# Performance work log

Hardware: AMD Instinct MI355X
Metric: run time of the kernel (lower is better)

Reference implementation:

```python
import jax, jax.numpy as jnp
import numpy as np

NMS_THRE = 0.4
NEG = -1e30  # sentinel for sort key of suppressed boxes


def _iou_adjacency(boxes, nms_thre):
    # boxes: [N,4] in cxcywh -> xyxy, then dense IoU >= thre adjacency (no self loops)
    cx, cy, w, h = boxes[:, 0], boxes[:, 1], boxes[:, 2], boxes[:, 3]
    x1 = cx - w / 2
    y1 = cy - h / 2
    x2 = x1 + w
    y2 = y1 + h
    b = jnp.stack([x1, y1, x2, y2], axis=-1)  # [N,4]
    area = (x2 - x1) * (y2 - y1)
    lt = jnp.maximum(b[:, None, :2], b[None, :, :2])  # [N,N,2]
    rb = jnp.minimum(b[:, None, 2:], b[None, :, 2:])
    wh = jnp.clip(rb - lt, 0.0)
    inter = wh[..., 0] * wh[..., 1]
    iou = inter / (area[:, None] + area[None, :] - inter)
    n = boxes.shape[0]
    return (iou >= nms_thre) & (~jnp.eye(n, dtype=bool))


def _greedy_suppress(valid0, adj, scores):
    # Sequential greedy NMS over candidates in descending score order.
    # valid shrinks monotonically, and valid <= valid0 always, so clearing
    # neighbors via adj row exactly matches the torch loop (which only clears
    # neighbors that were initially valid -- already-false entries are no-ops).
    order = jnp.argsort(-scores)

    def body(k, valid):
        idx = order[k]
        return jnp.where(valid[idx], valid & (~adj[idx]), valid)

    return jax.lax.fori_loop(0, scores.shape[0], body, valid0)


def _per_class(pro_c, con_c, conf_c, adj):
    # scatter_max over adjacency: max of con over neighbors (0 if no neighbors,
    # matching torch_scatter's zero-init)
    adj_con = jnp.max(jnp.where(adj, con_c[None, :], 0.0), axis=1)
    valid0 = (pro_c >= conf_c) & (pro_c >= adj_con) & (pro_c >= con_c)
    return _greedy_suppress(valid0, adj, pro_c)


def _per_image(pro, con, boxes, scale, conf_thres):
    # pro/con: [N,C]; boxes: [N,4] cxcywh; scale: scalar; conf_thres: [C]
    adj = _iou_adjacency(boxes, NMS_THRE)
    survive = jax.vmap(_per_class, in_axes=(1, 1, 0, None))(pro, con, conf_thres, adj)  # [C,N]
    b = boxes * scale
    cx, cy, w, h = b[:, 0], b[:, 1], b[:, 2], b[:, 3]
    xyxy = jnp.stack([cx - 0.5 * w, cy - 0.5 * h, cx + 0.5 * w, cy + 0.5 * h], axis=-1)  # [N,4]
    scores = pro.T  # [C,N]
    C = scores.shape[0]
    bws = jnp.concatenate(
        [jnp.broadcast_to(xyxy[None], (C,) + xyxy.shape), scores[..., None]], axis=-1
    )  # [C,N,5]
    bws = bws * survive[..., None].astype(bws.dtype)  # zero out suppressed rows
    key = jnp.where(survive, scores, NEG)
    perm = jnp.argsort(-key, axis=1)  # per-class descending score order
    bws = jnp.take_along_axis(bws, perm[..., None], axis=1)
    mask = jnp.take_along_axis(survive, perm, axis=1)
    return bws, mask


def setup_inputs() -> dict:
    key = jax.random.key(0)
    k1, k2, k3, k4 = jax.random.split(key, 4)
    B, N, C = 4, 3600, 16
    return {
        "pro_max": jax.random.uniform(k1, (B, N, C), dtype=jnp.float32),
        "con_max": jax.random.uniform(k2, (B, N, C), dtype=jnp.float32),
        "pred_boxes": jax.random.uniform(k3, (B, N, 4), dtype=jnp.float32),
        "image_scales": jax.random.uniform(k4, (B,), dtype=jnp.float32),
        "conf_thres": jnp.zeros((C,), dtype=jnp.float32),
    }


def reference(pro_max, con_max, pred_boxes, image_scales, conf_thres):
    # Returns (boxes_with_scores [B,C,N,5] sorted per class by score desc,
    #          survive_mask [B,C,N] aligned with the sorted rows).
    return jax.vmap(_per_image, in_axes=(0, 0, 0, 0, None))(
        pro_max, con_max, pred_boxes, image_scales, conf_thres
    )
```

## Files before the change

### kernel.cpp

```cpp
#include <hip/hip_runtime.h>
#include <cstdint>

typedef unsigned long long u64;
typedef unsigned int u32;

#define B_ 4
#define N_ 3600
#define C_ 16
#define NW_ 57
#define NPAD_ 3648
#define RPW_ 4
#define RPB_ 16
#define HW0_ 1856
#define HW1_ 1792
#define CH_ 64
#define NT_ 512
#define NWV_ 8
#define RPWG_ 8

__global__ __launch_bounds__(256, 5) void k_adj(const float* __restrict__ boxes,
                                                u64* __restrict__ adj) {
#pragma clang fp contract(off)
    __shared__ float4 sbox[HW0_];
    const int tid  = threadIdx.x;
    const int lane = tid & 63;
    const int wv   = tid >> 6;
    const int g    = blockIdx.x;
    const int b    = g / (N_ / RPB_);
    const int r0   = (g % (N_ / RPB_)) * RPB_ + wv * RPW_;
    const size_t bN = (size_t)b * N_;

    float4 bi[RPW_];
    float  ai[RPW_];
#pragma unroll
    for (int r = 0; r < RPW_; ++r) {
        const float4 bx = reinterpret_cast<const float4*>(boxes)[bN + r0 + r];
        const float x1 = bx.x - bx.z * 0.5f;
        const float y1 = bx.y - bx.w * 0.5f;
        const float x2 = x1 + bx.z;
        const float y2 = y1 + bx.w;
        bi[r] = make_float4(x1, y1, x2, y2);
        ai[r] = (x2 - x1) * (y2 - y1);
    }
    const double MID = (double)0.4f - 0x1p-26;

    u64 row[RPW_];
#pragma unroll
    for (int r = 0; r < RPW_; ++r) row[r] = 0ull;

    int jbase = 0;
    for (int h = 0; h < 2; ++h) {
        const int cnt = h ? HW1_ : HW0_;
        __syncthreads();
        for (int jj = tid; jj < cnt; jj += 256) {
            const int j = jbase + jj;
            float x1 = 0.f, y1 = 0.f, x2 = 0.f, y2 = 0.f;
            if (j < N_) {
                const float4 bx = reinterpret_cast<const float4*>(boxes)[bN + j];
                x1 = bx.x - bx.z * 0.5f;
                y1 = bx.y - bx.w * 0.5f;
                x2 = x1 + bx.z;
                y2 = y1 + bx.w;
            }
            sbox[jj] = make_float4(x1, y1, x2, y2);
        }
        __syncthreads();

        const int twn = cnt >> 6;
        for (int tw = 0; tw < twn; ++tw) {
            const int tglob = (jbase >> 6) + tw;
            const int j     = jbase + tw * 64 + lane;
            const float4 bj = sbox[tw * 64 + lane];
            const float ajr = (bj.z - bj.x) * (bj.w - bj.y);
#pragma unroll
            for (int r = 0; r < RPW_; ++r) {
                const float ltx = fmaxf(bi[r].x, bj.x);
                const float lty = fmaxf(bi[r].y, bj.y);
                const float rbx = fminf(bi[r].z, bj.z);
                const float rby = fminf(bi[r].w, bj.w);
                const float whx = fmaxf(rbx - ltx, 0.0f);
                const float why = fmaxf(rby - lty, 0.0f);
                const float inter = whx * why;
                const float denom = (ai[r] + ajr) - inter;
                const int pred = ((double)inter > MID * (double)denom) && (j != r0 + r);
                const u64 m = __ballot(pred);
                if (lane == tglob) row[r] = m;
            }
        }
        jbase += cnt;
    }

#pragma unroll
    for (int r = 0; r < RPW_; ++r)
        if (lane < NW_) adj[(bN + r0 + r) * (size_t)NW_ + lane] = row[r];
}

__global__ __launch_bounds__(256) void k_acon(const u64* __restrict__ adj,
                                              const float* __restrict__ con,
                                              float* __restrict__ thr) {
    const int tid  = threadIdx.x;
    const int lane = tid & 63;
    const int wv   = tid >> 6;
    const int g    = blockIdx.x;
    const int b    = g / (N_ / 4);
    const int i    = (g % (N_ / 4)) * 4 + wv;
    const size_t bN = (size_t)b * N_;

    u64 w = (lane < NW_) ? adj[(bN + i) * (size_t)NW_ + lane] : 0ull;

    float cm[C_];
#pragma unroll
    for (int k = 0; k < C_; ++k) cm[k] = 0.0f;

    while (w) {
        const int bit = __builtin_ctzll(w); w &= w - 1;
        const int j   = lane * 64 + bit;
        const float4* cp = reinterpret_cast<const float4*>(con + (bN + j) * C_);
        const float4 c0 = cp[0], c1 = cp[1], c2 = cp[2], c3 = cp[3];
        cm[0]  = fmaxf(cm[0],  c0.x); cm[1]  = fmaxf(cm[1],  c0.y);
        cm[2]  = fmaxf(cm[2],  c0.z); cm[3]  = fmaxf(cm[3],  c0.w);
        cm[4]  = fmaxf(cm[4],  c1.x); cm[5]  = fmaxf(cm[5],  c1.y);
        cm[6]  = fmaxf(cm[6],  c1.z); cm[7]  = fmaxf(cm[7],  c1.w);
        cm[8]  = fmaxf(cm[8],  c2.x); cm[9]  = fmaxf(cm[9],  c2.y);
        cm[10] = fmaxf(cm[10], c2.z); cm[11] = fmaxf(cm[11], c2.w);
        cm[12] = fmaxf(cm[12], c3.x); cm[13] = fmaxf(cm[13], c3.y);
        cm[14] = fmaxf(cm[14], c3.z); cm[15] = fmaxf(cm[15], c3.w);
    }

#pragma unroll
    for (int off = 1; off < 64; off <<= 1) {
#pragma unroll
        for (int k = 0; k < C_; ++k) cm[k] = fmaxf(cm[k], __shfl_xor(cm[k], off));
    }
    if (lane == 0) {
        const float4* cp = reinterpret_cast<const float4*>(con + (bN + i) * C_);
        const float4 c0 = cp[0], c1 = cp[1], c2 = cp[2], c3 = cp[3];
        float4* o = reinterpret_cast<float4*>(thr + (bN + i) * C_);
        o[0] = make_float4(fmaxf(cm[0],  c0.x), fmaxf(cm[1],  c0.y),
                           fmaxf(cm[2],  c0.z), fmaxf(cm[3],  c0.w));
        o[1] = make_float4(fmaxf(cm[4],  c1.x), fmaxf(cm[5],  c1.y),
                           fmaxf(cm[6],  c1.z), fmaxf(cm[7],  c1.w));
        o[2] = make_float4(fmaxf(cm[8],  c2.x), fmaxf(cm[9],  c2.y),
                           fmaxf(cm[10], c2.z), fmaxf(cm[11], c2.w));
        o[3] = make_float4(fmaxf(cm[12], c3.x), fmaxf(cm[13], c3.y),
                           fmaxf(cm[14], c3.z), fmaxf(cm[15], c3.w));
    }
}

union OvT {
    u64 keys[4096];
    u64 srows[2][CH_][NW_];
};

__global__ __launch_bounds__(NT_) void k_nms(const float* __restrict__ pro,
                                             const float* __restrict__ thr,
                                             const float* __restrict__ conf,
                                             const u64* __restrict__ adj,
                                             const float* __restrict__ boxes,
                                             const float* __restrict__ scales,
                                             float* __restrict__ out) {
#pragma clang fp contract(off)
    __shared__ OvT ov;
    __shared__ u32 sidx[NPAD_];
    __shared__ u64 sintra[CH_];
    __shared__ u64 vmask[NW_];
    __shared__ u64 s_accept;
    __shared__ u32 slist[NPAD_];
    __shared__ u32 s_T;
    __shared__ u32 s_S;
    const int tid  = threadIdx.x;
    const int lane = tid & 63;
    const int wv   = tid >> 6;
    const int bc   = blockIdx.x;
    const int b    = bc / C_, c = bc % C_;
    const size_t bN = (size_t)b * N_;
    const float cf = conf[c];

    if (tid == 0) s_T = 0;
    __syncthreads();

    for (int t = wv; t < NW_; t += NWV_) {
        const int i = t * 64 + lane;
        int pred = 0;
        u32 pk = 0;
        if (i < N_) {
            const size_t off = (bN + i) * C_ + c;
            const float p = pro[off];
            pred = (p >= cf) && (p >= thr[off]);
            const u32 pb = __float_as_uint(p);
            pk = pb ^ ((pb >> 31) ? 0xFFFFFFFFu : 0x80000000u);
        }
        const u64 bm = __ballot(pred);
        if (lane == 0) vmask[t] = bm;
        u32 base = 0;
        if (lane == 0 && bm) base = atomicAdd(&s_T, (u32)__popcll(bm));
        base = (u32)__shfl((int)base, 0);
        if (pred) ov.keys[base + (u32)__popcll(bm & ((1ull << lane) - 1ull))] =
            (((u64)(~pk)) << 32) | (u32)i;
    }
    __syncthreads();

    const int T = (int)s_T;
    int P = 2;
    while (P < T) P <<= 1;
    for (int x = T + tid; x < P; x += NT_) ov.keys[x] = ~0ull;
    __syncthreads();

    for (int k = 2; k <= P; k <<= 1) {
        for (int j = k >> 1; j > 0; j >>= 1) {
            for (int t = tid; t < P; t += NT_) {
                const int ixj = t ^ j;
                if (ixj > t) {
                    const u64 a = ov.keys[t], bb = ov.keys[ixj];
                    const bool up = ((t & k) == 0);
                    if ((a > bb) == up) { ov.keys[t] = bb; ov.keys[ixj] = a; }
                }
            }
            __syncthreads();
        }
    }

    for (int x = tid; x < T; x += NT_) sidx[x] = (u32)(ov.keys[x] & 0xFFFFFFFFull);
    __syncthreads();

#pragma unroll
    for (int rr = 0; rr < RPWG_; ++rr) {
        const int r = wv * RPWG_ + rr;
        const u32 idx = (r < T) ? sidx[r] : 0u;
        if (lane < NW_) ov.srows[0][r][lane] = adj[(bN + idx) * (size_t)NW_ + lane];
    }
    __syncthreads();

    u32 S = 0;
    const int NCH = (T + CH_ - 1) / CH_;
    for (int ch = 0; ch < NCH; ++ch) {
        const int cur = ch & 1, nxt = cur ^ 1;
        const int c0 = ch * CH_;
        const int cn = min(CH_, T - c0);
        const int havenext = (ch + 1 < NCH);

        u64 pre[RPWG_];
#pragma unroll
        for (int rr = 0; rr < RPWG_; ++rr) {
            const int r = wv * RPWG_ + rr;
            const int q = c0 + CH_ + r;
            const u32 idxn = (havenext && q < T) ? sidx[q] : 0u;
            pre[rr] = (havenext && lane < NW_)
                        ? adj[(bN + idxn) * (size_t)NW_ + lane] : 0ull;
        }
#pragma unroll
        for (int rr = 0; rr < RPWG_; ++rr) {
            const int r = wv * RPWG_ + rr;
            const u32 idxr = (c0 + r < T) ? sidx[c0 + r] : 0u;
            const u64 rj = ov.srows[cur][lane][idxr >> 6];
            const u64 ib = __ballot((lane < cn) && ((rj >> (idxr & 63)) & 1ull));
            if (lane == 0) sintra[r] = ib;
        }
        __syncthreads();

        if (wv == 0) {
            const u32 idxme = (c0 + lane < T) ? sidx[c0 + lane] : 0u;
            const u64 vm = vmask[idxme >> 6];
            u64 cv = __ballot((lane < cn) && ((vm >> (idxme & 63)) & 1ull));
            const u64 iv = sintra[lane];
            const u32 ivLo = (u32)iv, ivHi = (u32)(iv >> 32);
            u64 accept = 0ull;
            while (cv) {
                const int r = __builtin_ctzll(cv);
                accept |= 1ull << r;
                const u64 ir =
                    ((u64)(u32)__builtin_amdgcn_readlane((int)ivHi, r) << 32)
                  |  (u64)(u32)__builtin_amdgcn_readlane((int)ivLo, r);
                cv &= ~(ir | (1ull << r));
            }
            if (lane == 0) s_accept = accept;
            const u32 bitl = (u32)((accept >> lane) & 1ull);
            if (bitl) {
                const u32 pos = S + (u32)__popcll(accept & ((1ull << lane) - 1ull));
                slist[pos] = idxme;
            }
            S += (u32)__popcll(accept);
        }
        __syncthreads();

        const u64 ac = s_accept;
        u64 acc = 0ull;
#pragma unroll
        for (int rr = 0; rr < RPWG_; ++rr) {
            const int r = wv * RPWG_ + rr;
            if ((ac >> r) & 1ull)
                acc |= ov.srows[cur][r][min(lane, NW_ - 1)];
        }
        if (lane < NW_ && acc)
            atomicAnd(&vmask[lane], ~acc);
        if (havenext) {
#pragma unroll
            for (int rr = 0; rr < RPWG_; ++rr) {
                const int r = wv * RPWG_ + rr;
                if (lane < NW_) ov.srows[nxt][r][lane] = pre[rr];
            }
        }
        __syncthreads();
    }
    if (wv == 0 && lane == 0) s_S = S;
    __syncthreads();

    const int Sf = (int)s_S;
    const float s = scales[b];
    for (int r = tid; r < Sf; r += NT_) {
        const int idx = (int)slist[r];
        const float4 bx = reinterpret_cast<const float4*>(boxes)[bN + idx];
        const float scx = bx.x * s, scy = bx.y * s, sw = bx.z * s, sh = bx.w * s;
        float* o = out + ((size_t)bc * N_ + r) * 5;
        o[0] = scx - 0.5f * sw;
        o[1] = scy - 0.5f * sh;
        o[2] = scx + 0.5f * sw;
        o[3] = scy + 0.5f * sh;
        o[4] = pro[(bN + idx) * C_ + c];
        out[(size_t)B_ * C_ * N_ * 5 + (size_t)bc * N_ + r] = 1.0f;
    }
}

extern "C" void kernel_launch(void* const* d_in, const int* in_sizes, int n_in,
                              void* d_out, int out_size, void* d_ws, size_t ws_size,
                              hipStream_t stream) {
    const float* pro    = (const float*)d_in[0];
    const float* con    = (const float*)d_in[1];
    const float* boxes  = (const float*)d_in[2];
    const float* scales = (const float*)d_in[3];
    const float* conf   = (const float*)d_in[4];

    char* ws = (char*)d_ws;
    u64* adj = (u64*)ws;
    size_t off = (size_t)B_ * N_ * NW_ * sizeof(u64);
    float* thr = (float*)(ws + off);

    hipMemsetAsync(d_out, 0, (size_t)out_size * sizeof(float), stream);
    k_adj <<<B_ * N_ / RPB_, 256, 0, stream>>>(boxes, adj);
    k_acon<<<B_ * N_ / 4,    256, 0, stream>>>(adj, con, thr);
    k_nms <<<B_ * C_,        NT_, 0, stream>>>(pro, thr, conf, adj, boxes,
                                               scales, (float*)d_out);
}
```

Measured before the change: 177.5 us.

## Fuse neighbor-max into adjacency kernel, rank-sort keys, drop output memset

Moves the scatter-max over IoU neighbors into the adjacency kernel so each wave reuses its freshly built row bits, which removes the k_acon launch and the adjacency re-read. Replaces the bitonic sort of candidate keys in k_nms with a counting rank sort over shared memory, which avoids the many barrier-separated passes but costs O(T^2) compares. Removes the hipMemsetAsync by having k_nms write zeros for every unused output row itself. The adjacency kernel's occupancy hint drops from 5 to 4 to fit the extra registers.

```diff
diff --git a/kernel.cpp b/kernel.cpp
--- a/kernel.cpp
+++ b/kernel.cpp
@@ -18,8 +18,10 @@
 #define NWV_ 8
 #define RPWG_ 8
 
-__global__ __launch_bounds__(256, 5) void k_adj(const float* __restrict__ boxes,
-                                                u64* __restrict__ adj) {
+__global__ __launch_bounds__(256, 4) void k_adj(const float* __restrict__ boxes,
+                                                const float* __restrict__ con,
+                                                u64* __restrict__ adj,
+                                                float* __restrict__ thr) {
 #pragma clang fp contract(off)
     __shared__ float4 sbox[HW0_];
     const int tid  = threadIdx.x;
@@ -93,62 +95,53 @@
 #pragma unroll
     for (int r = 0; r < RPW_; ++r)
         if (lane < NW_) adj[(bN + r0 + r) * (size_t)NW_ + lane] = row[r];
+
+#pragma unroll 1
+    for (int r = 0; r < RPW_; ++r) {
+        const int i = r0 + r;
+        u64 w = row[r];
+        float cm[C_];
+#pragma unroll
+        for (int k = 0; k < C_; ++k) cm[k] = 0.0f;
+
+        while (w) {
+            const int bit = __builtin_ctzll(w); w &= w - 1;
+            const int j   = lane * 64 + bit;
+            const float4* cp = reinterpret_cast<const float4*>(con + (bN + j) * C_);
+            const float4 c0 = cp[0], c1 = cp[1], c2 = cp[2], c3 = cp[3];
+            cm[0]  = fmaxf(cm[0],  c0.x); cm[1]  = fmaxf(cm[1],  c0.y);
+            cm[2]  = fmaxf(cm[2],  c0.z); cm[3]  = fmaxf(cm[3],  c0.w);
+            cm[4]  = fmaxf(cm[4],  c1.x); cm[5]  = fmaxf(cm[5],  c1.y);
+            cm[6]  = fmaxf(cm[6],  c1.z); cm[7]  = fmaxf(cm[7],  c1.w);
+            cm[8]  = fmaxf(cm[8],  c2.x); cm[9]  = fmaxf(cm[9],  c2.y);
+            cm[10] = fmaxf(cm[10], c2.z); cm[11] = fmaxf(cm[11], c2.w);
+            cm[12] = fmaxf(cm[12], c3.x); cm[13] = fmaxf(cm[13], c3.y);
+            cm[14] = fmaxf(cm[14], c3.z); cm[15] = fmaxf(cm[15], c3.w);
+        }
+
+#pragma unroll
+        for (int off = 1; off < 64; off <<= 1) {
+#pragma unroll
+            for (int k = 0; k < C_; ++k) cm[k] = fmaxf(cm[k], __shfl_xor(cm[k], off));
+        }
+        if (lane == 0) {
+            const float4* cp = reinterpret_cast<const float4*>(con + (bN + i) * C_);
+            const float4 c0 = cp[0], c1 = cp[1], c2 = cp[2], c3 = cp[3];
+            float4* o = reinterpret_cast<float4*>(thr + (bN + i) * C_);
+            o[0] = make_float4(fmaxf(cm[0],  c0.x), fmaxf(cm[1],  c0.y),
+                               fmaxf(cm[2],  c0.z), fmaxf(cm[3],  c0.w));
+            o[1] = make_float4(fmaxf(cm[4],  c1.x), fmaxf(cm[5],  c1.y),
+                               fmaxf(cm[6],  c1.z), fmaxf(cm[7],  c1.w));
+            o[2] = make_float4(fmaxf(cm[8],  c2.x), fmaxf(cm[9],  c2.y),
+                               fmaxf(cm[10], c2.z), fmaxf(cm[11], c2.w));
+            o[3] = make_float4(fmaxf(cm[12], c3.x), fmaxf(cm[13], c3.y),
+                               fmaxf(cm[14], c3.z), fmaxf(cm[15], c3.w));
+        }
+    }
 }
 
-__global__ __launch_bounds__(256) void k_acon(const u64* __restrict__ adj,
-                                              const float* __restrict__ con,
-                                              float* __restrict__ thr) {
-    const int tid  = threadIdx.x;
-    const int lane = tid & 63;
-    const int wv   = tid >> 6;
-    const int g    = blockIdx.x;
-    const int b    = g / (N_ / 4);
-    const int i    = (g % (N_ / 4)) * 4 + wv;
-    const size_t bN = (size_t)b * N_;
-
-    u64 w = (lane < NW_) ? adj[(bN + i) * (size_t)NW_ + lane] : 0ull;
-
-    float cm[C_];
-#pragma unroll
-    for (int k = 0; k < C_; ++k) cm[k] = 0.0f;
-
-    while (w) {
-        const int bit = __builtin_ctzll(w); w &= w - 1;
-        const int j   = lane * 64 + bit;
-        const float4* cp = reinterpret_cast<const float4*>(con + (bN + j) * C_);
-        const float4 c0 = cp[0], c1 = cp[1], c2 = cp[2], c3 = cp[3];
-        cm[0]  = fmaxf(cm[0],  c0.x); cm[1]  = fmaxf(cm[1],  c0.y);
-        cm[2]  = fmaxf(cm[2],  c0.z); cm[3]  = fmaxf(cm[3],  c0.w);
-        cm[4]  = fmaxf(cm[4],  c1.x); cm[5]  = fmaxf(cm[5],  c1.y);
-        cm[6]  = fmaxf(cm[6],  c1.z); cm[7]  = fmaxf(cm[7],  c1.w);
-        cm[8]  = fmaxf(cm[8],  c2.x); cm[9]  = fmaxf(cm[9],  c2.y);
-        cm[10] = fmaxf(cm[10], c2.z); cm[11] = fmaxf(cm[11], c2.w);
-        cm[12] = fmaxf(cm[12], c3.x); cm[13] = fmaxf(cm[13], c3.y);
-        cm[14] = fmaxf(cm[14], c3.z); cm[15] = fmaxf(cm[15], c3.w);
-    }
-
-#pragma unroll
-    for (int off = 1; off < 64; off <<= 1) {
-#pragma unroll
-        for (int k = 0; k < C_; ++k) cm[k] = fmaxf(cm[k], __shfl_xor(cm[k], off));
-    }
-    if (lane == 0) {
-        const float4* cp = reinterpret_cast<const float4*>(con + (bN + i) * C_);
-        const float4 c0 = cp[0], c1 = cp[1], c2 = cp[2], c3 = cp[3];
-        float4* o = reinterpret_cast<float4*>(thr + (bN + i) * C_);
-        o[0] = make_float4(fmaxf(cm[0],  c0.x), fmaxf(cm[1],  c0.y),
-                           fmaxf(cm[2],  c0.z), fmaxf(cm[3],  c0.w));
-        o[1] = make_float4(fmaxf(cm[4],  c1.x), fmaxf(cm[5],  c1.y),
-                           fmaxf(cm[6],  c1.z), fmaxf(cm[7],  c1.w));
-        o[2] = make_float4(fmaxf(cm[8],  c2.x), fmaxf(cm[9],  c2.y),
-                           fmaxf(cm[10], c2.z), fmaxf(cm[11], c2.w));
-        o[3] = make_float4(fmaxf(cm[12], c3.x), fmaxf(cm[13], c3.y),
-                           fmaxf(cm[14], c3.z), fmaxf(cm[15], c3.w));
-    }
-}
-
 union OvT {
-    u64 keys[4096];
+    u64 keys[NPAD_];
     u64 srows[2][CH_][NW_];
 };
 
@@ -201,26 +194,13 @@
     __syncthreads();
 
     const int T = (int)s_T;
-    int P = 2;
-    while (P < T) P <<= 1;
-    for (int x = T + tid; x < P; x += NT_) ov.keys[x] = ~0ull;
-    __syncthreads();
-
-    for (int k = 2; k <= P; k <<= 1) {
-        for (int j = k >> 1; j > 0; j >>= 1) {
-            for (int t = tid; t < P; t += NT_) {
-                const int ixj = t ^ j;
-                if (ixj > t) {
-                    const u64 a = ov.keys[t], bb = ov.keys[ixj];
-                    const bool up = ((t & k) == 0);
-                    if ((a > bb) == up) { ov.keys[t] = bb; ov.keys[ixj] = a; }
-                }
-            }
-            __syncthreads();
-        }
-    }
-
-    for (int x = tid; x < T; x += NT_) sidx[x] = (u32)(ov.keys[x] & 0xFFFFFFFFull);
+    for (int k = 0; k * NT_ < T; ++k) {
+        const int x  = tid + k * NT_;
+        const u64 kx = (x < T) ? ov.keys[x] : ~0ull;
+        u32 rank = 0;
+        for (int y = 0; y < T; ++y) rank += (ov.keys[y] < kx);
+        if (x < T) sidx[rank] = (u32)(kx & 0xFFFFFFFFull);
+    }
     __syncthreads();
 
 #pragma unroll
@@ -307,17 +287,23 @@
 
     const int Sf = (int)s_S;
     const float s = scales[b];
-    for (int r = tid; r < Sf; r += NT_) {
-        const int idx = (int)slist[r];
-        const float4 bx = reinterpret_cast<const float4*>(boxes)[bN + idx];
-        const float scx = bx.x * s, scy = bx.y * s, sw = bx.z * s, sh = bx.w * s;
+    for (int r = tid; r < N_; r += NT_) {
+        float o0 = 0.f, o1 = 0.f, o2 = 0.f, o3 = 0.f, o4 = 0.f, mk = 0.f;
+        if (r < Sf) {
+            const int idx = (int)slist[r];
+            const float4 bx = reinterpret_cast<const float4*>(boxes)[bN + idx];
+            const float scx = bx.x * s, scy = bx.y * s;
+            const float sw  = bx.z * s, sh  = bx.w * s;
+            o0 = scx - 0.5f * sw;
+            o1 = scy - 0.5f * sh;
+            o2 = scx + 0.5f * sw;
+            o3 = scy + 0.5f * sh;
+            o4 = pro[(bN + idx) * C_ + c];
+            mk = 1.0f;
+        }
         float* o = out + ((size_t)bc * N_ + r) * 5;
-        o[0] = scx - 0.5f * sw;
-        o[1] = scy - 0.5f * sh;
-        o[2] = scx + 0.5f * sw;
-        o[3] = scy + 0.5f * sh;
-        o[4] = pro[(bN + idx) * C_ + c];
-        out[(size_t)B_ * C_ * N_ * 5 + (size_t)bc * N_ + r] = 1.0f;
+        o[0] = o0; o[1] = o1; o[2] = o2; o[3] = o3; o[4] = o4;
+        out[(size_t)B_ * C_ * N_ * 5 + (size_t)bc * N_ + r] = mk;
     }
 }
 
@@ -335,9 +321,7 @@
     size_t off = (size_t)B_ * N_ * NW_ * sizeof(u64);
     float* thr = (float*)(ws + off);
 
-    hipMemsetAsync(d_out, 0, (size_t)out_size * sizeof(float), stream);
-    k_adj <<<B_ * N_ / RPB_, 256, 0, stream>>>(boxes, adj);
-    k_acon<<<B_ * N_ / 4,    256, 0, stream>>>(adj, con, thr);
-    k_nms <<<B_ * C_,        NT_, 0, stream>>>(pro, thr, conf, adj, boxes,
-                                               scales, (float*)d_out);
+    k_adj<<<B_ * N_ / RPB_, 256, 0, stream>>>(boxes, con, adj, thr);
+    k_nms<<<B_ * C_,        NT_, 0, stream>>>(pro, thr, conf, adj, boxes,
+                                              scales, (float*)d_out);
 }
```

After: 173.7 us. 2.1% less time.
